# Performance work log

Measured on AMD Instinct MI355X. Metric: run time of the kernel, lower is better.

Reference implementation:

```python
import jax, jax.numpy as jnp
import numpy as np

B, L, D = 8, 1024, 512
H, DK, DV = 8, 64, 64
EPS = 1e-6
NEG = -1e9


def setup_inputs() -> dict:
    key = jax.random.key(0)
    ks = jax.random.split(key, 12)
    def xavier(k, shape):
        fan_out, fan_in = shape
        bound = float(np.sqrt(6.0 / (fan_in + fan_out)))
        return jax.random.uniform(k, shape, jnp.float32, -bound, bound)
    return {
        "q": jax.random.normal(ks[0], (B, L, D), jnp.float32),
        "k": jax.random.normal(ks[1], (B, L, D), jnp.float32),
        "v": jax.random.normal(ks[2], (B, L, D), jnp.float32),
        "event_type": jax.random.randint(ks[3], (B, L), 0, 2, jnp.int32),
        "mask": jax.random.randint(ks[4], (B, L, L), 0, 2, jnp.int32).astype(bool),
        "w_qs": xavier(ks[5], (H * DK, D)),
        "w_ex_en_qs": xavier(ks[6], (H * DK, D)),
        "w_ks": xavier(ks[7], (H * DK, D)),
        "w_vs": xavier(ks[8], (H * DV, D)),
        "w_fc": xavier(ks[9], (D, H * DV)),
        "b_fc": jnp.zeros((D,), jnp.float32),
        "ln_gamma": jnp.ones((D,), jnp.float32),
        "ln_beta": jnp.zeros((D,), jnp.float32),
    }


def _layer_norm(x, gamma, beta):
    mu = jnp.mean(x, axis=-1, keepdims=True)
    var = jnp.var(x, axis=-1, keepdims=True)
    return (x - mu) * jax.lax.rsqrt(var + EPS) * gamma + beta


def reference(q, k, v, event_type, mask, w_qs, w_ex_en_qs, w_ks, w_vs, w_fc, b_fc, ln_gamma, ln_beta):
    residual = q
    qn = _layer_norm(q, ln_gamma, ln_beta)  # normalize_before=True

    # event-type flags: en_en = prev is en AND present is en; ex_en = prev is ex AND present is en
    is_en = event_type != 0                                   # [B, L]
    en_en = (is_en[:, :, None] & is_en[:, None, :])[:, None]  # [B, 1, L, L]
    ex_en = ((~is_en)[:, :, None] & is_en[:, None, :])[:, None]

    def proj(x, w, d):  # torch Linear: x @ w.T, then split heads -> [B, H, L, d]
        return (x @ w.T).reshape(B, L, H, d).transpose(0, 2, 1, 3)

    q_en = proj(qn, w_qs, DK)
    q_ex = proj(qn, w_ex_en_qs, DK)
    kh = proj(k, w_ks, DK)
    vh = proj(v, w_vs, DV)

    temp = jnp.asarray(DK ** 0.5, qn.dtype)
    scores_en = jnp.einsum('bhqd,bhkd->bhqk', q_en / temp, kh)
    scores_en = jnp.where(mask[:, None], NEG, scores_en)      # masked branch
    scores_ex = jnp.einsum('bhqd,bhkd->bhqk', q_ex / temp, kh)  # unmasked branch

    blended = en_en * scores_en + ex_en * scores_ex           # [B, H, L, L]
    attn = jax.nn.softmax(blended, axis=-1)

    out = jnp.einsum('bhqk,bhkd->bhqd', attn, vh)             # PV
    out = out.transpose(0, 2, 1, 3).reshape(B, L, H * DV)
    out = out @ w_fc.T + b_fc
    out = out + residual
    return out, attn
```

## Files before the change

kernel.cpp:

```cpp
#include <hip/hip_runtime.h>

typedef __attribute__((ext_vector_type(8))) short bf16x8;
typedef __attribute__((ext_vector_type(4))) float f32x4;

#define DEVI static __device__ __forceinline__

constexpr float NEGV = -1e9f;

DEVI unsigned short f2b(float f) {
  union { float f; unsigned int u; } c; c.f = f;
  unsigned int lsb = (c.u >> 16) & 1u;
  return (unsigned short)((c.u + 0x7fffu + lsb) >> 16);
}
DEVI float sb2f(short s) {
  union { unsigned int u; float f; } c;
  c.u = ((unsigned int)(unsigned short)s) << 16;
  return c.f;
}

DEVI void gload16(const unsigned short* g, unsigned short* l) {
  __builtin_amdgcn_global_load_lds(
      (const __attribute__((address_space(1))) unsigned int*)g,
      (__attribute__((address_space(3))) unsigned int*)l, 16, 0, 0);
}

__global__ void mask_detect(const unsigned int* __restrict__ m, int n, int* flag) {
  unsigned int v = 0;
  for (int i = blockIdx.x * blockDim.x + threadIdx.x; i < n; i += gridDim.x * blockDim.x)
    v |= m[i];
  if (v & ~1u) atomicOr(flag, 1);
}

__global__ void mask_canon_bits(const void* __restrict__ mraw, unsigned int* __restrict__ mb,
                                int nwords, const int* __restrict__ flag) {
  int i = blockIdx.x * blockDim.x + threadIdx.x;
  if (i >= nwords) return;
  bool isbytes = (*flag != 0);
  unsigned int out = 0;
  if (isbytes) {
    const unsigned int* p = (const unsigned int*)mraw + (size_t)i * 8;
    #pragma unroll
    for (int w = 0; w < 8; w++) {
      unsigned int bw = p[w];
      out |= ((bw & 1u) << (w * 4)) | (((bw >> 8) & 1u) << (w * 4 + 1)) |
             (((bw >> 16) & 1u) << (w * 4 + 2)) | (((bw >> 24) & 1u) << (w * 4 + 3));
    }
  } else {
    const int4* p = (const int4*)mraw + (size_t)i * 8;
    #pragma unroll
    for (int w = 0; w < 8; w++) {
      int4 v = p[w];
      out |= ((v.x != 0 ? 1u : 0u) << (w * 4)) | ((v.y != 0 ? 1u : 0u) << (w * 4 + 1)) |
             ((v.z != 0 ? 1u : 0u) << (w * 4 + 2)) | ((v.w != 0 ? 1u : 0u) << (w * 4 + 3));
    }
  }
  mb[i] = out;
}

__global__ __launch_bounds__(256) void ln_kernel(const float* __restrict__ q,
    const float* __restrict__ gamma, const float* __restrict__ beta,
    unsigned short* __restrict__ qn) {
  int row = blockIdx.x;
  int t = threadIdx.x;
  const float* x = q + (size_t)row * 512;
  float2 v = reinterpret_cast<const float2*>(x)[t];
  float s = v.x + v.y, s2 = v.x * v.x + v.y * v.y;
  #pragma unroll
  for (int o = 32; o; o >>= 1) { s += __shfl_xor(s, o); s2 += __shfl_xor(s2, o); }
  __shared__ float ls[4], ls2[4];
  int w = t >> 6;
  if ((t & 63) == 0) { ls[w] = s; ls2[w] = s2; }
  __syncthreads();
  float S = ls[0] + ls[1] + ls[2] + ls[3];
  float S2 = ls2[0] + ls2[1] + ls2[2] + ls2[3];
  float mu = S * (1.f / 512.f);
  float var = S2 * (1.f / 512.f) - mu * mu;
  float r = rsqrtf(var + 1e-6f);
  float g0 = gamma[t * 2], g1 = gamma[t * 2 + 1];
  float b0 = beta[t * 2], b1 = beta[t * 2 + 1];
  ushort2 o;
  o.x = f2b((v.x - mu) * r * g0 + b0);
  o.y = f2b((v.y - mu) * r * g1 + b1);
  reinterpret_cast<ushort2*>(qn + (size_t)row * 512)[t] = o;
}

template<int MODE, bool CVX, bool CVW>
__global__ __launch_bounds__(256) void gemm_bt(
    const void* __restrict__ Xv,
    const void* __restrict__ Wv,
    void* __restrict__ Yv,
    float scale,
    const float* __restrict__ bias,
    const float* __restrict__ resid) {
  constexpr int LDT = 40;
  __shared__ __align__(16) unsigned short lA[64 * LDT];
  __shared__ __align__(16) unsigned short lB[64 * LDT];
  int t = threadIdx.x;
  int w = t >> 6, l = t & 63, lr = l & 15, lg = l >> 4;
  int mb = blockIdx.x * 64, nb = blockIdx.y * 64;
  f32x4 acc[4];
  #pragma unroll
  for (int n = 0; n < 4; n++) acc[n] = {0.f, 0.f, 0.f, 0.f};
  int sr = t >> 2, sc = (t & 3) * 8;
  for (int k0 = 0; k0 < 512; k0 += 32) {
    __syncthreads();
    if constexpr (CVX) {
      const float* src = (const float*)Xv + (size_t)(mb + sr) * 512 + k0 + sc;
      float4 x0 = *reinterpret_cast<const float4*>(src);
      float4 x1 = *reinterpret_cast<const float4*>(src + 4);
      ushort4 h0{f2b(x0.x), f2b(x0.y), f2b(x0.z), f2b(x0.w)};
      ushort4 h1{f2b(x1.x), f2b(x1.y), f2b(x1.z), f2b(x1.w)};
      *reinterpret_cast<ushort4*>(&lA[sr * LDT + sc]) = h0;
      *reinterpret_cast<ushort4*>(&lA[sr * LDT + sc + 4]) = h1;
    } else {
      *reinterpret_cast<float4*>(&lA[sr * LDT + sc]) =
          *reinterpret_cast<const float4*>((const unsigned short*)Xv + (size_t)(mb + sr) * 512 + k0 + sc);
    }
    if constexpr (CVW) {
      const float* src = (const float*)Wv + (size_t)(nb + sr) * 512 + k0 + sc;
      float4 x0 = *reinterpret_cast<const float4*>(src);
      float4 x1 = *reinterpret_cast<const float4*>(src + 4);
      ushort4 h0{f2b(x0.x), f2b(x0.y), f2b(x0.z), f2b(x0.w)};
      ushort4 h1{f2b(x1.x), f2b(x1.y), f2b(x1.z), f2b(x1.w)};
      *reinterpret_cast<ushort4*>(&lB[sr * LDT + sc]) = h0;
      *reinterpret_cast<ushort4*>(&lB[sr * LDT + sc + 4]) = h1;
    } else {
      *reinterpret_cast<float4*>(&lB[sr * LDT + sc]) =
          *reinterpret_cast<const float4*>((const unsigned short*)Wv + (size_t)(nb + sr) * 512 + k0 + sc);
    }
    __syncthreads();
    bf16x8 a = *reinterpret_cast<const bf16x8*>(&lA[(w * 16 + lr) * LDT + lg * 8]);
    #pragma unroll
    for (int n = 0; n < 4; n++) {
      bf16x8 bb = *reinterpret_cast<const bf16x8*>(&lB[(n * 16 + lr) * LDT + lg * 8]);
      acc[n] = __builtin_amdgcn_mfma_f32_16x16x32_bf16(a, bb, acc[n], 0, 0, 0);
    }
  }
  #pragma unroll
  for (int n = 0; n < 4; n++) {
    #pragma unroll
    for (int j = 0; j < 4; j++) {
      int m = mb + w * 16 + lg * 4 + j;
      int c = nb + n * 16 + lr;
      float val = acc[n][j] * scale;
      if constexpr (MODE == 0) {
        reinterpret_cast<unsigned short*>(Yv)[(size_t)m * 512 + c] = f2b(val);
      } else if constexpr (MODE == 1) {
        int bb_ = m >> 10, ll = m & 1023, hh = c >> 6, dd = c & 63;
        reinterpret_cast<unsigned short*>(Yv)[((size_t)((bb_ * 8 + hh) * 64 + dd)) * 1024 + ll] = f2b(val);
      } else {
        reinterpret_cast<float*>(Yv)[(size_t)m * 512 + c] =
            val + bias[c] + resid[(size_t)m * 512 + c];
      }
    }
  }
}

__global__ __launch_bounds__(256) void attn_kernel(
    const unsigned short* __restrict__ qen,
    const unsigned short* __restrict__ qex,
    const unsigned short* __restrict__ kh,
    const unsigned short* __restrict__ vhT,
    const int* __restrict__ etype,
    const unsigned int* __restrict__ mbits,
    float* __restrict__ attn_g,
    unsigned short* __restrict__ pv_out) {
  int qt = blockIdx.x, h = blockIdx.y, b = blockIdx.z;
  int t = threadIdx.x, w = t >> 6, l = t & 63, lr = l & 15, lg = l >> 4;
  __shared__ unsigned int ekbits[32];
  __shared__ unsigned int mkill[64 * 33];
  __shared__ __align__(16) unsigned short klds[2][2048];
  __shared__ __align__(16) unsigned short vlds[2][2048];
  __shared__ __align__(16) unsigned short pbuf[4][16][40];

  int qb = qt * 64 + w * 16;
  int qrowA = qb + lr;
  bool evA = etype[b * 1024 + qrowA] != 0;
  const unsigned short* qp = evA ? qen : qex;
  size_t qoff = (size_t)(b * 1024 + qrowA) * 512 + h * 64;
  bf16x8 a0 = *reinterpret_cast<const bf16x8*>(qp + qoff + lg * 8);
  bf16x8 a1 = *reinterpret_cast<const bf16x8*>(qp + qoff + 32 + lg * 8);

  if (t < 32) {
    unsigned int wdd = 0;
    const int4* ep = (const int4*)(etype + b * 1024 + t * 32);
    #pragma unroll
    for (int j4 = 0; j4 < 8; j4++) {
      int4 e = ep[j4];
      wdd |= ((e.x != 0 ? 1u : 0u) << (j4 * 4)) | ((e.y != 0 ? 1u : 0u) << (j4 * 4 + 1)) |
             ((e.z != 0 ? 1u : 0u) << (j4 * 4 + 2)) | ((e.w != 0 ? 1u : 0u) << (j4 * 4 + 3));
    }
    ekbits[t] = wdd;
  }
  {
    const unsigned int* mslice = mbits + ((size_t)(b * 1024 + qt * 64)) * 32;
    for (int i = t; i < 2048; i += 256) {
      int row = i >> 5, wd = i & 31;
      bool evq_row = etype[b * 1024 + qt * 64 + row] != 0;
      mkill[row * 33 + wd] = evq_row ? mslice[i] : 0u;
    }
  }

  int qrc[4], qlc[4];
  #pragma unroll
  for (int j = 0; j < 4; j++) { qlc[j] = w * 16 + lg * 4 + j; qrc[j] = qt * 64 + qlc[j]; }

  int srow = t >> 3, sb8 = t & 7;
  const unsigned short* kgsrc = kh + ((size_t)(b * 1024) + srow) * 512 + h * 64
                                + ((sb8 ^ (srow & 7)) << 3);
  unsigned short* kdst0 = &klds[0][(t & 192) * 8];
  unsigned short* kdst1 = &klds[1][(t & 192) * 8];
  int vrow = t >> 2, vb4 = t & 3;
  const unsigned short* vb_base = vhT + ((size_t)((b * 8 + h) * 64)) * 1024;
  const unsigned short* vgsrc = vb_base + (size_t)vrow * 1024 + ((vb4 ^ ((vrow >> 1) & 3)) << 3);
  unsigned short* vdst0 = &vlds[0][(t & 192) * 8];
  unsigned short* vdst1 = &vlds[1][(t & 192) * 8];

  gload16(kgsrc, kdst0);
  __syncthreads();

  float srun[4] = {0.f, 0.f, 0.f, 0.f};
  for (int c = 0; c < 32; c++) {
    int cur = c & 1;
    if (c < 31) gload16(kgsrc + (size_t)(c + 1) * 32 * 512, cur ? kdst0 : kdst1);
    #pragma unroll
    for (int c2 = 0; c2 < 2; c2++) {
      int kt = c * 2 + c2;
      int row = c2 * 16 + lr, r7 = row & 7;
      bf16x8 b0 = *reinterpret_cast<const bf16x8*>(&klds[cur][row * 64 + ((lg ^ r7) << 3)]);
      bf16x8 b1 = *reinterpret_cast<const bf16x8*>(&klds[cur][row * 64 + (((4 + lg) ^ r7) << 3)]);
      f32x4 cc = {0.f, 0.f, 0.f, 0.f};
      cc = __builtin_amdgcn_mfma_f32_16x16x32_bf16(a0, b0, cc, 0, 0, 0);
      cc = __builtin_amdgcn_mfma_f32_16x16x32_bf16(a1, b1, cc, 0, 0, 0);
      int wcol = kt >> 1, bitpos = ((kt & 1) << 4) + lr;
      bool ekb = (ekbits[wcol] >> bitpos) & 1;
      #pragma unroll
      for (int j = 0; j < 4; j++) {
        bool mk = (mkill[qlc[j] * 33 + wcol] >> bitpos) & 1;
        float val = ekb ? (mk ? NEGV : cc[j]) : 0.f;
        srun[j] += __expf(val);
      }
    }
    __syncthreads();
  }
  float rS[4];
  #pragma unroll
  for (int j = 0; j < 4; j++) {
    float s = srun[j];
    s += __shfl_xor(s, 1); s += __shfl_xor(s, 2);
    s += __shfl_xor(s, 4); s += __shfl_xor(s, 8);
    rS[j] = 1.f / s;
  }

  f32x4 oacc[4];
  #pragma unroll
  for (int n = 0; n < 4; n++) oacc[n] = {0.f, 0.f, 0.f, 0.f};
  float* ag = attn_g + ((size_t)(b * 8 + h)) * 1024 * 1024;
  float* agrow = ag + (size_t)(qb + lr) * 1024 + lg * 8;

  gload16(kgsrc, kdst0);
  gload16(vgsrc, vdst0);
  __syncthreads();

  for (int c = 0; c < 32; c++) {
    int cur = c & 1;
    if (c < 31) {
      gload16(kgsrc + (size_t)(c + 1) * 32 * 512, cur ? kdst0 : kdst1);
      gload16(vgsrc + (size_t)(c + 1) * 32, cur ? vdst0 : vdst1);
    }
    #pragma unroll
    for (int c2 = 0; c2 < 2; c2++) {
      int kt = c * 2 + c2;
      int row = c2 * 16 + lr, r7 = row & 7;
      bf16x8 b0 = *reinterpret_cast<const bf16x8*>(&klds[cur][row * 64 + ((lg ^ r7) << 3)]);
      bf16x8 b1 = *reinterpret_cast<const bf16x8*>(&klds[cur][row * 64 + (((4 + lg) ^ r7) << 3)]);
      f32x4 cc = {0.f, 0.f, 0.f, 0.f};
      cc = __builtin_amdgcn_mfma_f32_16x16x32_bf16(a0, b0, cc, 0, 0, 0);
      cc = __builtin_amdgcn_mfma_f32_16x16x32_bf16(a1, b1, cc, 0, 0, 0);
      int wcol = kt >> 1, bitpos = ((kt & 1) << 4) + lr;
      bool ekb = (ekbits[wcol] >> bitpos) & 1;
      #pragma unroll
      for (int j = 0; j < 4; j++) {
        bool mk = (mkill[qlc[j] * 33 + wcol] >> bitpos) & 1;
        float val = ekb ? (mk ? NEGV : cc[j]) : 0.f;
        float p = __expf(val) * rS[j];
        pbuf[w][lg * 4 + j][(c2 << 4) + lr] = f2b(p);
      }
      if (c2) {
        bf16x8 pa = *reinterpret_cast<const bf16x8*>(&pbuf[w][lr][lg * 8]);
        f32x4 f0, f1;
        f0[0] = sb2f(pa[0]); f0[1] = sb2f(pa[1]); f0[2] = sb2f(pa[2]); f0[3] = sb2f(pa[3]);
        f1[0] = sb2f(pa[4]); f1[1] = sb2f(pa[5]); f1[2] = sb2f(pa[6]); f1[3] = sb2f(pa[7]);
        __builtin_nontemporal_store(f0, reinterpret_cast<f32x4*>(agrow + c * 32));
        __builtin_nontemporal_store(f1, reinterpret_cast<f32x4*>(agrow + c * 32 + 4));
        #pragma unroll
        for (int n = 0; n < 4; n++) {
          int vr = n * 16 + lr;
          int cb = (lg ^ ((vr >> 1) & 3)) << 3;
          bf16x8 vb = *reinterpret_cast<const bf16x8*>(&vlds[cur][vr * 32 + cb]);
          oacc[n] = __builtin_amdgcn_mfma_f32_16x16x32_bf16(pa, vb, oacc[n], 0, 0, 0);
        }
      }
    }
    __syncthreads();
  }
  #pragma unroll
  for (int n = 0; n < 4; n++) {
    #pragma unroll
    for (int j = 0; j < 4; j++) {
      __builtin_nontemporal_store(f2b(oacc[n][j]),
          &pv_out[(size_t)(b * 1024 + qrc[j]) * 512 + h * 64 + n * 16 + lr]);
    }
  }
}

extern "C" void kernel_launch(void* const* d_in, const int* in_sizes, int n_in,
                              void* d_out, int out_size, void* d_ws, size_t ws_size,
                              hipStream_t stream) {
  (void)in_sizes; (void)n_in; (void)out_size; (void)ws_size;
  const float* q     = (const float*)d_in[0];
  const float* k     = (const float*)d_in[1];
  const float* v     = (const float*)d_in[2];
  const int* etype   = (const int*)d_in[3];
  const void* mask_raw = d_in[4];
  const float* w_qs  = (const float*)d_in[5];
  const float* w_ex  = (const float*)d_in[6];
  const float* w_ks  = (const float*)d_in[7];
  const float* w_vs  = (const float*)d_in[8];
  const float* w_fc  = (const float*)d_in[9];
  const float* b_fc  = (const float*)d_in[10];
  const float* gamma = (const float*)d_in[11];
  const float* beta  = (const float*)d_in[12];

  char* ws = (char*)d_ws;
  const size_t MB = 1024 * 1024;
  unsigned short* qn   = (unsigned short*)(ws);
  unsigned short* qen  = (unsigned short*)(ws + 8 * MB);
  unsigned short* qex  = (unsigned short*)(ws + 16 * MB);
  unsigned short* khb  = (unsigned short*)(ws + 24 * MB);
  unsigned short* vhT  = (unsigned short*)(ws + 32 * MB);
  unsigned short* ao   = (unsigned short*)(ws + 40 * MB);
  unsigned int* mbits  = (unsigned int*)(ws + 48 * MB);
  int* mflag           = (int*)(ws + 49 * MB);

  float* outp = (float*)d_out;
  float* attn_g = outp + (size_t)8 * 1024 * 512;

  ln_kernel<<<8192, 256, 0, stream>>>(q, gamma, beta, qn);

  const int MASK_N = 8 * 1024 * 1024;
  hipMemsetAsync(mflag, 0, 4, stream);
  mask_detect<<<2048, 256, 0, stream>>>((const unsigned int*)mask_raw, MASK_N / 4, mflag);
  const int NWORDS = MASK_N / 32;
  mask_canon_bits<<<(NWORDS + 255) / 256, 256, 0, stream>>>(mask_raw, mbits, NWORDS, mflag);

  dim3 gg(128, 8);
  gemm_bt<0, false, true><<<gg, 256, 0, stream>>>(qn, w_qs, qen, 0.125f, nullptr, nullptr);
  gemm_bt<0, false, true><<<gg, 256, 0, stream>>>(qn, w_ex, qex, 0.125f, nullptr, nullptr);
  gemm_bt<0, true,  true><<<gg, 256, 0, stream>>>(k,  w_ks, khb, 1.0f, nullptr, nullptr);
  gemm_bt<1, true,  true><<<gg, 256, 0, stream>>>(v,  w_vs, vhT, 1.0f, nullptr, nullptr);

  attn_kernel<<<dim3(16, 8, 8), 256, 0, stream>>>(qen, qex, khb, vhT, etype, mbits,
                                                  attn_g, ao);

  gemm_bt<2, false, true><<<gg, 256, 0, stream>>>(ao, w_fc, outp, 1.0f, b_fc, q);
}
```

Baseline: 264.3 us.

## Batch four projection GEMMs into one launch with larger 128x128 tiles

The four Q/K/V projection GEMMs now run as a single kernel launch, with blockIdx.z choosing the weight and output. The output-projection GEMM gets its own kernel. Both move from 64x64 tiles with one A-fragment per wave to 128x128 tiles where each wave computes a 4x4 grid of MFMA fragments, which raises register-level reuse and cuts global reloads of the weights and activations. The cost is more registers per thread and fewer blocks (1024 for the fused projections, 256 for fc), which may hurt occupancy, especially in the fc launch.

```diff
diff --git a/kernel.cpp b/kernel.cpp
--- a/kernel.cpp
+++ b/kernel.cpp
@@ -84,73 +84,146 @@
   reinterpret_cast<ushort2*>(qn + (size_t)row * 512)[t] = o;
 }
 
-template<int MODE, bool CVX, bool CVW>
-__global__ __launch_bounds__(256) void gemm_bt(
-    const void* __restrict__ Xv,
-    const void* __restrict__ Wv,
-    void* __restrict__ Yv,
-    float scale,
-    const float* __restrict__ bias,
-    const float* __restrict__ resid) {
+__global__ __launch_bounds__(256) void proj_gemm(
+    const unsigned short* __restrict__ qn, const float* __restrict__ kf,
+    const float* __restrict__ vf,
+    const float* __restrict__ w_qs, const float* __restrict__ w_ex,
+    const float* __restrict__ w_ks, const float* __restrict__ w_vs,
+    unsigned short* __restrict__ qen, unsigned short* __restrict__ qex,
+    unsigned short* __restrict__ khb, unsigned short* __restrict__ vhT) {
   constexpr int LDT = 40;
-  __shared__ __align__(16) unsigned short lA[64 * LDT];
-  __shared__ __align__(16) unsigned short lB[64 * LDT];
-  int t = threadIdx.x;
-  int w = t >> 6, l = t & 63, lr = l & 15, lg = l >> 4;
-  int mb = blockIdx.x * 64, nb = blockIdx.y * 64;
-  f32x4 acc[4];
-  #pragma unroll
-  for (int n = 0; n < 4; n++) acc[n] = {0.f, 0.f, 0.f, 0.f};
-  int sr = t >> 2, sc = (t & 3) * 8;
+  __shared__ __align__(16) unsigned short lA[128 * LDT];
+  __shared__ __align__(16) unsigned short lB[128 * LDT];
+  int z = blockIdx.z;
+  const float* W = (z == 0) ? w_qs : (z == 1) ? w_ex : (z == 2) ? w_ks : w_vs;
+  float scale = (z < 2) ? 0.125f : 1.0f;
+  int t = threadIdx.x, w = t >> 6, l = t & 63, lr = l & 15, lg = l >> 4;
+  int wr = w >> 1, wc = w & 1;
+  int mt = blockIdx.x * 128, nt = blockIdx.y * 128;
+  f32x4 acc[4][4];
+  #pragma unroll
+  for (int i = 0; i < 4; i++)
+    #pragma unroll
+    for (int jj = 0; jj < 4; jj++) acc[i][jj] = {0.f, 0.f, 0.f, 0.f};
+  int sr = t >> 1, sc = (t & 1) * 16;
   for (int k0 = 0; k0 < 512; k0 += 32) {
     __syncthreads();
-    if constexpr (CVX) {
-      const float* src = (const float*)Xv + (size_t)(mb + sr) * 512 + k0 + sc;
-      float4 x0 = *reinterpret_cast<const float4*>(src);
-      float4 x1 = *reinterpret_cast<const float4*>(src + 4);
-      ushort4 h0{f2b(x0.x), f2b(x0.y), f2b(x0.z), f2b(x0.w)};
-      ushort4 h1{f2b(x1.x), f2b(x1.y), f2b(x1.z), f2b(x1.w)};
-      *reinterpret_cast<ushort4*>(&lA[sr * LDT + sc]) = h0;
-      *reinterpret_cast<ushort4*>(&lA[sr * LDT + sc + 4]) = h1;
+    if (z < 2) {
+      const unsigned short* src = qn + (size_t)(mt + sr) * 512 + k0 + sc;
+      *reinterpret_cast<float4*>(&lA[sr * LDT + sc]) =
+          *reinterpret_cast<const float4*>(src);
+      *reinterpret_cast<float4*>(&lA[sr * LDT + sc + 8]) =
+          *reinterpret_cast<const float4*>(src + 8);
     } else {
+      const float* src = ((z == 2) ? kf : vf) + (size_t)(mt + sr) * 512 + k0 + sc;
+      #pragma unroll
+      for (int i = 0; i < 4; i++) {
+        float4 x = *reinterpret_cast<const float4*>(src + i * 4);
+        ushort4 hh{f2b(x.x), f2b(x.y), f2b(x.z), f2b(x.w)};
+        *reinterpret_cast<ushort4*>(&lA[sr * LDT + sc + i * 4]) = hh;
+      }
+    }
+    {
+      const float* src = W + (size_t)(nt + sr) * 512 + k0 + sc;
+      #pragma unroll
+      for (int i = 0; i < 4; i++) {
+        float4 x = *reinterpret_cast<const float4*>(src + i * 4);
+        ushort4 hh{f2b(x.x), f2b(x.y), f2b(x.z), f2b(x.w)};
+        *reinterpret_cast<ushort4*>(&lB[sr * LDT + sc + i * 4]) = hh;
+      }
+    }
+    __syncthreads();
+    bf16x8 aF[4], bF[4];
+    #pragma unroll
+    for (int ai = 0; ai < 4; ai++)
+      aF[ai] = *reinterpret_cast<const bf16x8*>(&lA[(wr * 64 + ai * 16 + lr) * LDT + lg * 8]);
+    #pragma unroll
+    for (int bj = 0; bj < 4; bj++)
+      bF[bj] = *reinterpret_cast<const bf16x8*>(&lB[(wc * 64 + bj * 16 + lr) * LDT + lg * 8]);
+    #pragma unroll
+    for (int ai = 0; ai < 4; ai++)
+      #pragma unroll
+      for (int bj = 0; bj < 4; bj++)
+        acc[ai][bj] = __builtin_amdgcn_mfma_f32_16x16x32_bf16(aF[ai], bF[bj], acc[ai][bj], 0, 0, 0);
+  }
+  unsigned short* Y = (z == 0) ? qen : (z == 1) ? qex : (z == 2) ? khb : vhT;
+  #pragma unroll
+  for (int ai = 0; ai < 4; ai++) {
+    #pragma unroll
+    for (int bj = 0; bj < 4; bj++) {
+      #pragma unroll
+      for (int j = 0; j < 4; j++) {
+        int m = mt + wr * 64 + ai * 16 + lg * 4 + j;
+        int c = nt + wc * 64 + bj * 16 + lr;
+        unsigned short o = f2b(acc[ai][bj][j] * scale);
+        if (z < 3) {
+          Y[(size_t)m * 512 + c] = o;
+        } else {
+          int bb_ = m >> 10, ll = m & 1023, hh = c >> 6, dd = c & 63;
+          Y[((size_t)((bb_ * 8 + hh) * 64 + dd)) * 1024 + ll] = o;
+        }
+      }
+    }
+  }
+}
+
+__global__ __launch_bounds__(256) void fc_gemm(
+    const unsigned short* __restrict__ ao, const float* __restrict__ w_fc,
+    const float* __restrict__ bias, const float* __restrict__ resid,
+    float* __restrict__ out) {
+  constexpr int LDT = 40;
+  __shared__ __align__(16) unsigned short lA[128 * LDT];
+  __shared__ __align__(16) unsigned short lB[128 * LDT];
+  int t = threadIdx.x, w = t >> 6, l = t & 63, lr = l & 15, lg = l >> 4;
+  int wr = w >> 1, wc = w & 1;
+  int mt = blockIdx.x * 128, nt = blockIdx.y * 128;
+  f32x4 acc[4][4];
+  #pragma unroll
+  for (int i = 0; i < 4; i++)
+    #pragma unroll
+    for (int jj = 0; jj < 4; jj++) acc[i][jj] = {0.f, 0.f, 0.f, 0.f};
+  int sr = t >> 1, sc = (t & 1) * 16;
+  for (int k0 = 0; k0 < 512; k0 += 32) {
+    __syncthreads();
+    {
+      const unsigned short* src = ao + (size_t)(mt + sr) * 512 + k0 + sc;
       *reinterpret_cast<float4*>(&lA[sr * LDT + sc]) =
-          *reinterpret_cast<const float4*>((const unsigned short*)Xv + (size_t)(mb + sr) * 512 + k0 + sc);
-    }
-    if constexpr (CVW) {
-      const float* src = (const float*)Wv + (size_t)(nb + sr) * 512 + k0 + sc;
-      float4 x0 = *reinterpret_cast<const float4*>(src);
-      float4 x1 = *reinterpret_cast<const float4*>(src + 4);
-      ushort4 h0{f2b(x0.x), f2b(x0.y), f2b(x0.z), f2b(x0.w)};
-      ushort4 h1{f2b(x1.x), f2b(x1.y), f2b(x1.z), f2b(x1.w)};
-      *reinterpret_cast<ushort4*>(&lB[sr * LDT + sc]) = h0;
-      *reinterpret_cast<ushort4*>(&lB[sr * LDT + sc + 4]) = h1;
-    } else {
-      *reinterpret_cast<float4*>(&lB[sr * LDT + sc]) =
-          *reinterpret_cast<const float4*>((const unsigned short*)Wv + (size_t)(nb + sr) * 512 + k0 + sc);
-    }
-    __syncthreads();
-    bf16x8 a = *reinterpret_cast<const bf16x8*>(&lA[(w * 16 + lr) * LDT + lg * 8]);
-    #pragma unroll
-    for (int n = 0; n < 4; n++) {
-      bf16x8 bb = *reinterpret_cast<const bf16x8*>(&lB[(n * 16 + lr) * LDT + lg * 8]);
-      acc[n] = __builtin_amdgcn_mfma_f32_16x16x32_bf16(a, bb, acc[n], 0, 0, 0);
-    }
-  }
-  #pragma unroll
-  for (int n = 0; n < 4; n++) {
-    #pragma unroll
-    for (int j = 0; j < 4; j++) {
-      int m = mb + w * 16 + lg * 4 + j;
-      int c = nb + n * 16 + lr;
-      float val = acc[n][j] * scale;
-      if constexpr (MODE == 0) {
-        reinterpret_cast<unsigned short*>(Yv)[(size_t)m * 512 + c] = f2b(val);
-      } else if constexpr (MODE == 1) {
-        int bb_ = m >> 10, ll = m & 1023, hh = c >> 6, dd = c & 63;
-        reinterpret_cast<unsigned short*>(Yv)[((size_t)((bb_ * 8 + hh) * 64 + dd)) * 1024 + ll] = f2b(val);
-      } else {
-        reinterpret_cast<float*>(Yv)[(size_t)m * 512 + c] =
-            val + bias[c] + resid[(size_t)m * 512 + c];
+          *reinterpret_cast<const float4*>(src);
+      *reinterpret_cast<float4*>(&lA[sr * LDT + sc + 8]) =
+          *reinterpret_cast<const float4*>(src + 8);
+    }
+    {
+      const float* src = w_fc + (size_t)(nt + sr) * 512 + k0 + sc;
+      #pragma unroll
+      for (int i = 0; i < 4; i++) {
+        float4 x = *reinterpret_cast<const float4*>(src + i * 4);
+        ushort4 hh{f2b(x.x), f2b(x.y), f2b(x.z), f2b(x.w)};
+        *reinterpret_cast<ushort4*>(&lB[sr * LDT + sc + i * 4]) = hh;
+      }
+    }
+    __syncthreads();
+    bf16x8 aF[4], bF[4];
+    #pragma unroll
+    for (int ai = 0; ai < 4; ai++)
+      aF[ai] = *reinterpret_cast<const bf16x8*>(&lA[(wr * 64 + ai * 16 + lr) * LDT + lg * 8]);
+    #pragma unroll
+    for (int bj = 0; bj < 4; bj++)
+      bF[bj] = *reinterpret_cast<const bf16x8*>(&lB[(wc * 64 + bj * 16 + lr) * LDT + lg * 8]);
+    #pragma unroll
+    for (int ai = 0; ai < 4; ai++)
+      #pragma unroll
+      for (int bj = 0; bj < 4; bj++)
+        acc[ai][bj] = __builtin_amdgcn_mfma_f32_16x16x32_bf16(aF[ai], bF[bj], acc[ai][bj], 0, 0, 0);
+  }
+  #pragma unroll
+  for (int ai = 0; ai < 4; ai++) {
+    #pragma unroll
+    for (int bj = 0; bj < 4; bj++) {
+      #pragma unroll
+      for (int j = 0; j < 4; j++) {
+        int m = mt + wr * 64 + ai * 16 + lg * 4 + j;
+        int c = nt + wc * 64 + bj * 16 + lr;
+        out[(size_t)m * 512 + c] = acc[ai][bj][j] + bias[c] + resid[(size_t)m * 512 + c];
       }
     }
   }
@@ -354,14 +427,11 @@
   const int NWORDS = MASK_N / 32;
   mask_canon_bits<<<(NWORDS + 255) / 256, 256, 0, stream>>>(mask_raw, mbits, NWORDS, mflag);
 
-  dim3 gg(128, 8);
-  gemm_bt<0, false, true><<<gg, 256, 0, stream>>>(qn, w_qs, qen, 0.125f, nullptr, nullptr);
-  gemm_bt<0, false, true><<<gg, 256, 0, stream>>>(qn, w_ex, qex, 0.125f, nullptr, nullptr);
-  gemm_bt<0, true,  true><<<gg, 256, 0, stream>>>(k,  w_ks, khb, 1.0f, nullptr, nullptr);
-  gemm_bt<1, true,  true><<<gg, 256, 0, stream>>>(v,  w_vs, vhT, 1.0f, nullptr, nullptr);
+  proj_gemm<<<dim3(64, 4, 4), 256, 0, stream>>>(qn, k, v, w_qs, w_ex, w_ks, w_vs,
+                                                qen, qex, khb, vhT);
 
   attn_kernel<<<dim3(16, 8, 8), 256, 0, stream>>>(qen, qex, khb, vhT, etype, mbits,
                                                   attn_g, ao);
 
-  gemm_bt<2, false, true><<<gg, 256, 0, stream>>>(ao, w_fc, outp, 1.0f, b_fc, q);
-}
+  fc_gemm<<<dim3(64, 4), 256, 0, stream>>>(ao, w_fc, b_fc, q, outp);
+}
```

Measured after the change: 263.3 us. Within noise of the previous version (-0.4%).

## Fuse two-pass softmax into single pass with deferred normalization

Applied to the files above, without the earlier changes.

The separate row-sum pass that recomputed QK^T is removed. The kernel now does one pass that accumulates exp sums and the unnormalized P@V together, keeps the bf16 exp values packed in 128 registers per thread, and normalizes both the output and the stored attention matrix at the end. This drops half the QK MFMA and K loads but raises register pressure sharply, and launch_bounds(256,2) may force spills. Attention values are now rounded to bf16 before normalization instead of after, and there is no max subtraction, which relies on scores being small.

```diff
diff --git a/kernel.cpp b/kernel.cpp
--- a/kernel.cpp
+++ b/kernel.cpp
@@ -156,7 +156,7 @@
   }
 }
 
-__global__ __launch_bounds__(256) void attn_kernel(
+__global__ __launch_bounds__(256, 2) void attn_kernel(
     const unsigned short* __restrict__ qen,
     const unsigned short* __restrict__ qex,
     const unsigned short* __restrict__ kh,
@@ -172,6 +172,7 @@
   __shared__ __align__(16) unsigned short klds[2][2048];
   __shared__ __align__(16) unsigned short vlds[2][2048];
   __shared__ __align__(16) unsigned short pbuf[4][16][40];
+  __shared__ float rslds[4][16];
 
   int qb = qt * 64 + w * 16;
   int qrowA = qb + lr;
@@ -216,13 +217,23 @@
   unsigned short* vdst0 = &vlds[0][(t & 192) * 8];
   unsigned short* vdst1 = &vlds[1][(t & 192) * 8];
 
+  float srun[4] = {0.f, 0.f, 0.f, 0.f};
+  f32x4 oacc[4];
+  #pragma unroll
+  for (int n = 0; n < 4; n++) oacc[n] = {0.f, 0.f, 0.f, 0.f};
+  unsigned int ppk[32][4];
+
   gload16(kgsrc, kdst0);
+  gload16(vgsrc, vdst0);
   __syncthreads();
 
-  float srun[4] = {0.f, 0.f, 0.f, 0.f};
+  #pragma unroll
   for (int c = 0; c < 32; c++) {
     int cur = c & 1;
-    if (c < 31) gload16(kgsrc + (size_t)(c + 1) * 32 * 512, cur ? kdst0 : kdst1);
+    if (c < 31) {
+      gload16(kgsrc + (size_t)(c + 1) * 32 * 512, cur ? kdst0 : kdst1);
+      gload16(vgsrc + (size_t)(c + 1) * 32, cur ? vdst0 : vdst1);
+    }
     #pragma unroll
     for (int c2 = 0; c2 < 2; c2++) {
       int kt = c * 2 + c2;
@@ -238,61 +249,15 @@
       for (int j = 0; j < 4; j++) {
         bool mk = (mkill[qlc[j] * 33 + wcol] >> bitpos) & 1;
         float val = ekb ? (mk ? NEGV : cc[j]) : 0.f;
-        srun[j] += __expf(val);
-      }
-    }
-    __syncthreads();
-  }
-  float rS[4];
-  #pragma unroll
-  for (int j = 0; j < 4; j++) {
-    float s = srun[j];
-    s += __shfl_xor(s, 1); s += __shfl_xor(s, 2);
-    s += __shfl_xor(s, 4); s += __shfl_xor(s, 8);
-    rS[j] = 1.f / s;
-  }
-
-  f32x4 oacc[4];
-  #pragma unroll
-  for (int n = 0; n < 4; n++) oacc[n] = {0.f, 0.f, 0.f, 0.f};
-  float* ag = attn_g + ((size_t)(b * 8 + h)) * 1024 * 1024;
-  float* agrow = ag + (size_t)(qb + lr) * 1024 + lg * 8;
-
-  gload16(kgsrc, kdst0);
-  gload16(vgsrc, vdst0);
-  __syncthreads();
-
-  for (int c = 0; c < 32; c++) {
-    int cur = c & 1;
-    if (c < 31) {
-      gload16(kgsrc + (size_t)(c + 1) * 32 * 512, cur ? kdst0 : kdst1);
-      gload16(vgsrc + (size_t)(c + 1) * 32, cur ? vdst0 : vdst1);
-    }
-    #pragma unroll
-    for (int c2 = 0; c2 < 2; c2++) {
-      int kt = c * 2 + c2;
-      int row = c2 * 16 + lr, r7 = row & 7;
-      bf16x8 b0 = *reinterpret_cast<const bf16x8*>(&klds[cur][row * 64 + ((lg ^ r7) << 3)]);
-      bf16x8 b1 = *reinterpret_cast<const bf16x8*>(&klds[cur][row * 64 + (((4 + lg) ^ r7) << 3)]);
-      f32x4 cc = {0.f, 0.f, 0.f, 0.f};
-      cc = __builtin_amdgcn_mfma_f32_16x16x32_bf16(a0, b0, cc, 0, 0, 0);
-      cc = __builtin_amdgcn_mfma_f32_16x16x32_bf16(a1, b1, cc, 0, 0, 0);
-      int wcol = kt >> 1, bitpos = ((kt & 1) << 4) + lr;
-      bool ekb = (ekbits[wcol] >> bitpos) & 1;
-      #pragma unroll
-      for (int j = 0; j < 4; j++) {
-        bool mk = (mkill[qlc[j] * 33 + wcol] >> bitpos) & 1;
-        float val = ekb ? (mk ? NEGV : cc[j]) : 0.f;
-        float p = __expf(val) * rS[j];
-        pbuf[w][lg * 4 + j][(c2 << 4) + lr] = f2b(p);
+        float e = __expf(val);
+        srun[j] += e;
+        unsigned short us = f2b(e);
+        if (c2 == 0) ppk[c][j] = us;
+        else ppk[c][j] |= ((unsigned int)us) << 16;
+        pbuf[w][lg * 4 + j][(c2 << 4) + lr] = us;
       }
       if (c2) {
         bf16x8 pa = *reinterpret_cast<const bf16x8*>(&pbuf[w][lr][lg * 8]);
-        f32x4 f0, f1;
-        f0[0] = sb2f(pa[0]); f0[1] = sb2f(pa[1]); f0[2] = sb2f(pa[2]); f0[3] = sb2f(pa[3]);
-        f1[0] = sb2f(pa[4]); f1[1] = sb2f(pa[5]); f1[2] = sb2f(pa[6]); f1[3] = sb2f(pa[7]);
-        __builtin_nontemporal_store(f0, reinterpret_cast<f32x4*>(agrow + c * 32));
-        __builtin_nontemporal_store(f1, reinterpret_cast<f32x4*>(agrow + c * 32 + 4));
         #pragma unroll
         for (int n = 0; n < 4; n++) {
           int vr = n * 16 + lr;
@@ -304,13 +269,49 @@
     }
     __syncthreads();
   }
+
+  float rS[4];
+  #pragma unroll
+  for (int j = 0; j < 4; j++) {
+    float s = srun[j];
+    s += __shfl_xor(s, 1); s += __shfl_xor(s, 2);
+    s += __shfl_xor(s, 4); s += __shfl_xor(s, 8);
+    rS[j] = 1.f / s;
+  }
+  if (lr == 0) {
+    #pragma unroll
+    for (int j = 0; j < 4; j++) rslds[w][lg * 4 + j] = rS[j];
+  }
+
   #pragma unroll
   for (int n = 0; n < 4; n++) {
     #pragma unroll
     for (int j = 0; j < 4; j++) {
-      __builtin_nontemporal_store(f2b(oacc[n][j]),
+      __builtin_nontemporal_store(f2b(oacc[n][j] * rS[j]),
           &pv_out[(size_t)(b * 1024 + qrc[j]) * 512 + h * 64 + n * 16 + lr]);
     }
+  }
+  __syncthreads();
+  float rSl = rslds[w][lr];
+
+  float* ag = attn_g + ((size_t)(b * 8 + h)) * 1024 * 1024;
+  float* agrow = ag + (size_t)(qb + lr) * 1024 + lg * 8;
+  #pragma unroll
+  for (int c = 0; c < 32; c++) {
+    #pragma unroll
+    for (int j = 0; j < 4; j++) {
+      unsigned int pk = ppk[c][j];
+      pbuf[w][lg * 4 + j][lr] = (unsigned short)(pk & 0xffffu);
+      pbuf[w][lg * 4 + j][16 + lr] = (unsigned short)(pk >> 16);
+    }
+    bf16x8 pa = *reinterpret_cast<const bf16x8*>(&pbuf[w][lr][lg * 8]);
+    f32x4 f0, f1;
+    f0[0] = sb2f(pa[0]) * rSl; f0[1] = sb2f(pa[1]) * rSl;
+    f0[2] = sb2f(pa[2]) * rSl; f0[3] = sb2f(pa[3]) * rSl;
+    f1[0] = sb2f(pa[4]) * rSl; f1[1] = sb2f(pa[5]) * rSl;
+    f1[2] = sb2f(pa[6]) * rSl; f1[3] = sb2f(pa[7]) * rSl;
+    __builtin_nontemporal_store(f0, reinterpret_cast<f32x4*>(agrow + c * 32));
+    __builtin_nontemporal_store(f1, reinterpret_cast<f32x4*>(agrow + c * 32 + 4));
   }
 }
 
```

Result: slower. 411.6 us (+55.8%).
